# Kernel optimization log

Measured on AMD Instinct MI355X. Metric: run time of the kernel, lower is better.

## Reference

```python
import jax, jax.numpy as jnp
import numpy as np


def setup_inputs() -> dict:
    key = jax.random.key(0)
    k1, k2, k3, k4 = jax.random.split(key, 4)
    N, K, F, E = 50000, 32, 128, 16
    nodes = jax.random.normal(k1, (N, F), dtype=jnp.float32)
    nlist = jax.random.randint(k2, (N, K), 0, N, dtype=jnp.int64)
    edges = jax.random.uniform(k3, (N, K, E), dtype=jnp.float32)
    w = jax.random.normal(k4, (F, F, E), dtype=jnp.float32) * 0.05
    return {"nodes": nodes, "nlist": nlist, "edges": edges, "w": w}


def reference(nodes, nlist, edges, w):
    # gather neighbor features: [N, K, F]
    sliced = nodes[nlist]
    K = nlist.shape[1]
    # fused 3-way contraction + mean over neighbors (axis j):
    # original: einsum('ijn,ijl,lmn->ijm', edges, sliced, w).mean(axis=1)
    out = jnp.einsum('ijn,ijl,lmn->im', edges, sliced, w) / K
    return out
```

## Files before the change

kernel.cpp:

```cpp
#include <hip/hip_runtime.h>


typedef _Float16 half8  __attribute__((ext_vector_type(8)));
typedef _Float16 half4v __attribute__((ext_vector_type(4)));
typedef float    float4v __attribute__((ext_vector_type(4)));
typedef int      int4v  __attribute__((ext_vector_type(4)));
typedef unsigned int uint;

#define NF 128
#define NK 32
#define NE 16
#define RPB 32

__global__ __launch_bounds__(256) void k_prep_nodes(const float* __restrict__ src,
                                                    _Float16* __restrict__ dst, int n4) {
    int i = blockIdx.x * 256 + threadIdx.x;
    if (i < n4) {
        float4v v = ((const float4v*)src)[i];
        half4v h;
        h[0] = (_Float16)v[0]; h[1] = (_Float16)v[1];
        h[2] = (_Float16)v[2]; h[3] = (_Float16)v[3];
        ((half4v*)dst)[i] = h;
    }
}

__global__ __launch_bounds__(256) void k_prep_w(const float* __restrict__ w,
                                                _Float16* __restrict__ w2t) {
    int o  = blockIdx.x * 256 + threadIdx.x;
    int m  = o >> 11;
    int cf = o & 2047;
    int ch = cf >> 9;
    int cp = cf & 511;
    int ltq = cp >> 6;
    int n   = (cp >> 2) & 15;
    int g   = cp & 3;
    int l = ch * 32 + (ltq >> 2) * 16 + (ltq & 3) * 4 + g;
    w2t[o] = (_Float16)w[(l * NF + m) * NE + n];
}

__global__ __launch_bounds__(256, 4) void k_mp(const _Float16* __restrict__ nodes_h,
                                               const int* __restrict__ nlist,
                                               const float* __restrict__ edges,
                                               const _Float16* __restrict__ w2t,
                                               float* __restrict__ out, int N) {
    __shared__ __align__(16) _Float16 s_T[RPB * 512];
    __shared__ __align__(16) _Float16 s_G[4 * NK * 32];

    const int tid  = threadIdx.x;
    const int wv   = tid >> 6;
    const int ln   = tid & 63;
    const int quad = ln >> 4;
    const int c16  = ln & 15;
    const int row0 = blockIdx.x * RPB;

    _Float16* __restrict__ gbuf = &s_G[wv * (NK * 32)];
    const float4v zf = {0.f, 0.f, 0.f, 0.f};

    half8 fe[8];
    #pragma unroll
    for (int r = 0; r < 8; ++r) {
        int rg = row0 + wv * 8 + r; if (rg > N - 1) rg = N - 1;
        const float* ep = edges + (size_t)rg * (NK * NE) + quad * (8 * NE) + c16;
        #pragma unroll
        for (int jj = 0; jj < 8; ++jj) fe[r][jj] = (_Float16)ep[jj * NE];
    }

    const int jlane = ln >> 2;
    const int sub   = ln & 3;
    int nb0[8], nb1[8];
    #pragma unroll
    for (int r = 0; r < 8; ++r) {
        int rg = row0 + wv * 8 + r; if (rg > N - 1) rg = N - 1;
        nb0[r] = nlist[rg * NK + jlane]      << 8;
        nb1[r] = nlist[rg * NK + 16 + jlane] << 8;
    }
    const int wblk0 = (sub ^ ((jlane >> 3) & 3)) << 3;
    const int wblk1 = (sub ^ (((jlane + 16) >> 3) & 3)) << 3;

    float4v a00 = zf, a01 = zf, a10 = zf, a11 = zf;
    const char* nbase = (const char*)nodes_h;

    half8 p0 = *(const half8*)(nbase + nb0[0] + sub * 16);
    half8 p1 = *(const half8*)(nbase + nb1[0] + sub * 16);

    for (int ch = 0; ch < 4; ++ch) {
        #pragma unroll
        for (int r = 0; r < 8; ++r) {
            const int il = wv * 8 + r;
            half8 g0 = p0;
            half8 g1 = p1;
            if (r < 7) {
                p0 = *(const half8*)(nbase + nb0[r + 1] + ch * 64 + sub * 16);
                p1 = *(const half8*)(nbase + nb1[r + 1] + ch * 64 + sub * 16);
            }
            *(half8*)&gbuf[jlane * 32 + wblk0]        = g0;
            *(half8*)&gbuf[(jlane + 16) * 32 + wblk1] = g1;
            #pragma unroll
            for (int lt = 0; lt < 2; ++lt) {
                const int col   = lt * 16 + c16;
                const int rbase = quad * (8 * 32) + (col ^ (quad << 3));
                uint t0 = *(const unsigned short*)&gbuf[rbase + 0 * 32];
                uint t1 = *(const unsigned short*)&gbuf[rbase + 1 * 32];
                uint t2 = *(const unsigned short*)&gbuf[rbase + 2 * 32];
                uint t3 = *(const unsigned short*)&gbuf[rbase + 3 * 32];
                uint t4 = *(const unsigned short*)&gbuf[rbase + 4 * 32];
                uint t5 = *(const unsigned short*)&gbuf[rbase + 5 * 32];
                uint t6 = *(const unsigned short*)&gbuf[rbase + 6 * 32];
                uint t7 = *(const unsigned short*)&gbuf[rbase + 7 * 32];
                int4v pv;
                pv[0] = (int)(t0 | (t1 << 16));
                pv[1] = (int)(t2 | (t3 << 16));
                pv[2] = (int)(t4 | (t5 << 16));
                pv[3] = (int)(t6 | (t7 << 16));
                half8 av = __builtin_bit_cast(half8, pv);
                float4v d = __builtin_amdgcn_mfma_f32_16x16x32_f16(av, fe[r], zf, 0, 0, 0);
                const int ltq  = lt * 4 + quad;
                const int cb   = ltq * 64 + c16 * 4;
                const int phys = cb ^ ((((ltq ^ il) & 7)) << 3);
                half4v hv;
                hv[0] = (_Float16)d[0]; hv[1] = (_Float16)d[1];
                hv[2] = (_Float16)d[2]; hv[3] = (_Float16)d[3];
                *(half4v*)&s_T[il * 512 + phys] = hv;
            }
        }
        __syncthreads();

        if (ch < 3) {
            p0 = *(const half8*)(nbase + nb0[0] + (ch + 1) * 64 + sub * 16);
            p1 = *(const half8*)(nbase + nb1[0] + (ch + 1) * 64 + sub * 16);
        }

        const _Float16* wr0 = w2t + ((size_t)(wv * 2 + 0) * 16 + c16) * 2048 + ch * 512;
        const _Float16* wr1 = w2t + ((size_t)(wv * 2 + 1) * 16 + c16) * 2048 + ch * 512;
        #pragma unroll 4
        for (int kt = 0; kt < 16; ++kt) {
            const int cb2  = kt * 32 + quad * 8;
            const int mask = (((cb2 >> 6) ^ c16) & 7) << 3;
            half8 t0 = *(const half8*)&s_T[c16 * 512        + (cb2 ^ mask)];
            half8 t1 = *(const half8*)&s_T[(16 + c16) * 512 + (cb2 ^ mask)];
            half8 b0 = *(const half8*)(wr0 + cb2);
            half8 b1 = *(const half8*)(wr1 + cb2);
            a00 = __builtin_amdgcn_mfma_f32_16x16x32_f16(t0, b0, a00, 0, 0, 0);
            a10 = __builtin_amdgcn_mfma_f32_16x16x32_f16(t1, b0, a10, 0, 0, 0);
            a01 = __builtin_amdgcn_mfma_f32_16x16x32_f16(t0, b1, a01, 0, 0, 0);
            a11 = __builtin_amdgcn_mfma_f32_16x16x32_f16(t1, b1, a11, 0, 0, 0);
        }
        __syncthreads();
    }

    const float sc = 1.0f / (float)NK;
    const int mb = (wv << 5) + c16;
    #pragma unroll
    for (int g = 0; g < 4; ++g) {
        int i0 = row0 + quad * 4 + g;
        int i1 = i0 + 16;
        if (i0 < N) {
            out[(size_t)i0 * NF + mb]      = a00[g] * sc;
            out[(size_t)i0 * NF + mb + 16] = a01[g] * sc;
        }
        if (i1 < N) {
            out[(size_t)i1 * NF + mb]      = a10[g] * sc;
            out[(size_t)i1 * NF + mb + 16] = a11[g] * sc;
        }
    }
}

extern "C" void kernel_launch(void* const* d_in, const int* in_sizes, int n_in,
                              void* d_out, int out_size, void* d_ws, size_t ws_size,
                              hipStream_t stream) {
    const float* nodes = (const float*)d_in[0];
    const int*   nlist = (const int*)d_in[1];
    const float* edges = (const float*)d_in[2];
    const float* w     = (const float*)d_in[3];
    float* out = (float*)d_out;

    const int N = in_sizes[0] / NF;

    _Float16* w2t     = (_Float16*)d_ws;
    _Float16* nodes_h = (_Float16*)((char*)d_ws + 524288);

    const int n4 = (N * NF) / 4;
    k_prep_nodes<<<(n4 + 255) / 256, 256, 0, stream>>>(nodes, nodes_h, n4);
    k_prep_w<<<(NF * NF * NE) / 256, 256, 0, stream>>>(w, w2t);

    const int blocks = (N + RPB - 1) / RPB;
    k_mp<<<blocks, 256, 0, stream>>>(nodes_h, nlist, edges, w2t, out, N);
}
```

Baseline: 334.9 us.

## Halve rows per block, widen feature chunks, and stage output through LDS

The fused gather/MFMA kernel now handles 16 rows per block instead of 32. It processes features in two 64-wide chunks instead of four 32-wide chunks, with the weight reorder kernel changed to match. The gather layout moves to 8 lanes per neighbour row with four loads in flight, and the second-stage GEMM loop doubles in length with half the accumulators. Output goes through shared memory for coalesced float4 stores. This reduces barriers and gives more blocks for load balance, but each block reads the weight matrix for half as many rows, which doubles weight traffic per output. Occupancy hint drops to 3 blocks per CU.

```diff
diff --git a/kernel.cpp b/kernel.cpp
--- a/kernel.cpp
+++ b/kernel.cpp
@@ -10,7 +10,7 @@
 #define NF 128
 #define NK 32
 #define NE 16
-#define RPB 32
+#define RPB 16
 
 __global__ __launch_bounds__(256) void k_prep_nodes(const float* __restrict__ src,
                                                     _Float16* __restrict__ dst, int n4) {
@@ -26,25 +26,25 @@
 
 __global__ __launch_bounds__(256) void k_prep_w(const float* __restrict__ w,
                                                 _Float16* __restrict__ w2t) {
-    int o  = blockIdx.x * 256 + threadIdx.x;
-    int m  = o >> 11;
-    int cf = o & 2047;
-    int ch = cf >> 9;
-    int cp = cf & 511;
+    int o   = blockIdx.x * 256 + threadIdx.x;
+    int m   = o >> 11;
+    int cf  = o & 2047;
+    int ch  = cf >> 10;
+    int cp  = cf & 1023;
     int ltq = cp >> 6;
     int n   = (cp >> 2) & 15;
     int g   = cp & 3;
-    int l = ch * 32 + (ltq >> 2) * 16 + (ltq & 3) * 4 + g;
+    int l = ch * 64 + (ltq >> 2) * 16 + (ltq & 3) * 4 + g;
     w2t[o] = (_Float16)w[(l * NF + m) * NE + n];
 }
 
-__global__ __launch_bounds__(256, 4) void k_mp(const _Float16* __restrict__ nodes_h,
+__global__ __launch_bounds__(256, 3) void k_mp(const _Float16* __restrict__ nodes_h,
                                                const int* __restrict__ nlist,
                                                const float* __restrict__ edges,
                                                const _Float16* __restrict__ w2t,
                                                float* __restrict__ out, int N) {
-    __shared__ __align__(16) _Float16 s_T[RPB * 512];
-    __shared__ __align__(16) _Float16 s_G[4 * NK * 32];
+    __shared__ __align__(16) _Float16 s_T[RPB * 1024];
+    __shared__ __align__(16) _Float16 s_G[4 * 2048];
 
     const int tid  = threadIdx.x;
     const int wv   = tid >> 6;
@@ -53,60 +53,72 @@
     const int c16  = ln & 15;
     const int row0 = blockIdx.x * RPB;
 
-    _Float16* __restrict__ gbuf = &s_G[wv * (NK * 32)];
+    _Float16* __restrict__ gbuf = &s_G[wv * 2048];
     const float4v zf = {0.f, 0.f, 0.f, 0.f};
 
-    half8 fe[8];
-    #pragma unroll
-    for (int r = 0; r < 8; ++r) {
-        int rg = row0 + wv * 8 + r; if (rg > N - 1) rg = N - 1;
+    half8 fe[4];
+    #pragma unroll
+    for (int r = 0; r < 4; ++r) {
+        int rg = row0 + wv * 4 + r; if (rg > N - 1) rg = N - 1;
         const float* ep = edges + (size_t)rg * (NK * NE) + quad * (8 * NE) + c16;
         #pragma unroll
         for (int jj = 0; jj < 8; ++jj) fe[r][jj] = (_Float16)ep[jj * NE];
     }
 
-    const int jlane = ln >> 2;
-    const int sub   = ln & 3;
-    int nb0[8], nb1[8];
-    #pragma unroll
-    for (int r = 0; r < 8; ++r) {
-        int rg = row0 + wv * 8 + r; if (rg > N - 1) rg = N - 1;
-        nb0[r] = nlist[rg * NK + jlane]      << 8;
-        nb1[r] = nlist[rg * NK + 16 + jlane] << 8;
-    }
-    const int wblk0 = (sub ^ ((jlane >> 3) & 3)) << 3;
-    const int wblk1 = (sub ^ (((jlane + 16) >> 3) & 3)) << 3;
-
-    float4v a00 = zf, a01 = zf, a10 = zf, a11 = zf;
-    const char* nbase = (const char*)nodes_h;
-
-    half8 p0 = *(const half8*)(nbase + nb0[0] + sub * 16);
-    half8 p1 = *(const half8*)(nbase + nb1[0] + sub * 16);
-
-    for (int ch = 0; ch < 4; ++ch) {
+    const int jrow = ln >> 3;
+    const int s8   = ln & 7;
+    int nb0[4], nb1[4], nb2[4], nb3[4];
+    #pragma unroll
+    for (int r = 0; r < 4; ++r) {
+        int rg = row0 + wv * 4 + r; if (rg > N - 1) rg = N - 1;
+        const int* np = nlist + rg * NK + jrow;
+        nb0[r] = np[0]  << 8;
+        nb1[r] = np[8]  << 8;
+        nb2[r] = np[16] << 8;
+        nb3[r] = np[24] << 8;
+    }
+    const char* nbase = (const char*)nodes_h + (s8 << 4);
+
+    const int wo0 = (0 * 8 + jrow) * 64 + ((s8 ^ 0) << 3);
+    const int wo1 = (1 * 8 + jrow) * 64 + ((s8 ^ 1) << 3);
+    const int wo2 = (2 * 8 + jrow) * 64 + ((s8 ^ 2) << 3);
+    const int wo3 = (3 * 8 + jrow) * 64 + ((s8 ^ 3) << 3);
+
+    float4v a00 = zf, a01 = zf;
+
+    half8 pf0 = *(const half8*)(nbase + nb0[0]);
+    half8 pf1 = *(const half8*)(nbase + nb1[0]);
+    half8 pf2 = *(const half8*)(nbase + nb2[0]);
+    half8 pf3 = *(const half8*)(nbase + nb3[0]);
+
+    for (int ch = 0; ch < 2; ++ch) {
+        const int chb = ch << 7;
+
         #pragma unroll
-        for (int r = 0; r < 8; ++r) {
-            const int il = wv * 8 + r;
-            half8 g0 = p0;
-            half8 g1 = p1;
-            if (r < 7) {
-                p0 = *(const half8*)(nbase + nb0[r + 1] + ch * 64 + sub * 16);
-                p1 = *(const half8*)(nbase + nb1[r + 1] + ch * 64 + sub * 16);
+        for (int r = 0; r < 4; ++r) {
+            half8 g0 = pf0, g1 = pf1, g2 = pf2, g3 = pf3;
+            if (r < 3) {
+                pf0 = *(const half8*)(nbase + nb0[r + 1] + chb);
+                pf1 = *(const half8*)(nbase + nb1[r + 1] + chb);
+                pf2 = *(const half8*)(nbase + nb2[r + 1] + chb);
+                pf3 = *(const half8*)(nbase + nb3[r + 1] + chb);
             }
-            *(half8*)&gbuf[jlane * 32 + wblk0]        = g0;
-            *(half8*)&gbuf[(jlane + 16) * 32 + wblk1] = g1;
+            *(half8*)&gbuf[wo0] = g0;
+            *(half8*)&gbuf[wo1] = g1;
+            *(half8*)&gbuf[wo2] = g2;
+            *(half8*)&gbuf[wo3] = g3;
+            const int il = wv * 4 + r;
             #pragma unroll
-            for (int lt = 0; lt < 2; ++lt) {
-                const int col   = lt * 16 + c16;
-                const int rbase = quad * (8 * 32) + (col ^ (quad << 3));
-                uint t0 = *(const unsigned short*)&gbuf[rbase + 0 * 32];
-                uint t1 = *(const unsigned short*)&gbuf[rbase + 1 * 32];
-                uint t2 = *(const unsigned short*)&gbuf[rbase + 2 * 32];
-                uint t3 = *(const unsigned short*)&gbuf[rbase + 3 * 32];
-                uint t4 = *(const unsigned short*)&gbuf[rbase + 4 * 32];
-                uint t5 = *(const unsigned short*)&gbuf[rbase + 5 * 32];
-                uint t6 = *(const unsigned short*)&gbuf[rbase + 6 * 32];
-                uint t7 = *(const unsigned short*)&gbuf[rbase + 7 * 32];
+            for (int lt = 0; lt < 4; ++lt) {
+                const int rbase = quad * 512 + ((lt * 16 + c16) ^ (quad << 3));
+                uint t0 = *(const unsigned short*)&gbuf[rbase + 0 * 64];
+                uint t1 = *(const unsigned short*)&gbuf[rbase + 1 * 64];
+                uint t2 = *(const unsigned short*)&gbuf[rbase + 2 * 64];
+                uint t3 = *(const unsigned short*)&gbuf[rbase + 3 * 64];
+                uint t4 = *(const unsigned short*)&gbuf[rbase + 4 * 64];
+                uint t5 = *(const unsigned short*)&gbuf[rbase + 5 * 64];
+                uint t6 = *(const unsigned short*)&gbuf[rbase + 6 * 64];
+                uint t7 = *(const unsigned short*)&gbuf[rbase + 7 * 64];
                 int4v pv;
                 pv[0] = (int)(t0 | (t1 << 16));
                 pv[1] = (int)(t2 | (t3 << 16));
@@ -116,52 +128,52 @@
                 float4v d = __builtin_amdgcn_mfma_f32_16x16x32_f16(av, fe[r], zf, 0, 0, 0);
                 const int ltq  = lt * 4 + quad;
                 const int cb   = ltq * 64 + c16 * 4;
-                const int phys = cb ^ ((((ltq ^ il) & 7)) << 3);
+                const int phys = cb ^ (((ltq ^ il) & 7) << 3);
                 half4v hv;
                 hv[0] = (_Float16)d[0]; hv[1] = (_Float16)d[1];
                 hv[2] = (_Float16)d[2]; hv[3] = (_Float16)d[3];
-                *(half4v*)&s_T[il * 512 + phys] = hv;
+                *(half4v*)&s_T[il * 1024 + phys] = hv;
             }
         }
         __syncthreads();
 
-        if (ch < 3) {
-            p0 = *(const half8*)(nbase + nb0[0] + (ch + 1) * 64 + sub * 16);
-            p1 = *(const half8*)(nbase + nb1[0] + (ch + 1) * 64 + sub * 16);
+        if (ch == 0) {
+            pf0 = *(const half8*)(nbase + nb0[0] + 128);
+            pf1 = *(const half8*)(nbase + nb1[0] + 128);
+            pf2 = *(const half8*)(nbase + nb2[0] + 128);
+            pf3 = *(const half8*)(nbase + nb3[0] + 128);
         }
 
-        const _Float16* wr0 = w2t + ((size_t)(wv * 2 + 0) * 16 + c16) * 2048 + ch * 512;
-        const _Float16* wr1 = w2t + ((size_t)(wv * 2 + 1) * 16 + c16) * 2048 + ch * 512;
+        const _Float16* wr0 = w2t + ((size_t)(wv * 2 + 0) * 16 + c16) * 2048 + ch * 1024;
+        const _Float16* wr1 = w2t + ((size_t)(wv * 2 + 1) * 16 + c16) * 2048 + ch * 1024;
         #pragma unroll 4
-        for (int kt = 0; kt < 16; ++kt) {
+        for (int kt = 0; kt < 32; ++kt) {
             const int cb2  = kt * 32 + quad * 8;
             const int mask = (((cb2 >> 6) ^ c16) & 7) << 3;
-            half8 t0 = *(const half8*)&s_T[c16 * 512        + (cb2 ^ mask)];
-            half8 t1 = *(const half8*)&s_T[(16 + c16) * 512 + (cb2 ^ mask)];
+            half8 t0 = *(const half8*)&s_T[c16 * 1024 + (cb2 ^ mask)];
             half8 b0 = *(const half8*)(wr0 + cb2);
             half8 b1 = *(const half8*)(wr1 + cb2);
             a00 = __builtin_amdgcn_mfma_f32_16x16x32_f16(t0, b0, a00, 0, 0, 0);
-            a10 = __builtin_amdgcn_mfma_f32_16x16x32_f16(t1, b0, a10, 0, 0, 0);
             a01 = __builtin_amdgcn_mfma_f32_16x16x32_f16(t0, b1, a01, 0, 0, 0);
-            a11 = __builtin_amdgcn_mfma_f32_16x16x32_f16(t1, b1, a11, 0, 0, 0);
         }
         __syncthreads();
     }
 
+    float* sf = (float*)s_T;
     const float sc = 1.0f / (float)NK;
     const int mb = (wv << 5) + c16;
     #pragma unroll
     for (int g = 0; g < 4; ++g) {
-        int i0 = row0 + quad * 4 + g;
-        int i1 = i0 + 16;
-        if (i0 < N) {
-            out[(size_t)i0 * NF + mb]      = a00[g] * sc;
-            out[(size_t)i0 * NF + mb + 16] = a01[g] * sc;
-        }
-        if (i1 < N) {
-            out[(size_t)i1 * NF + mb]      = a10[g] * sc;
-            out[(size_t)i1 * NF + mb + 16] = a11[g] * sc;
-        }
+        sf[(quad * 4 + g) * NF + mb]      = a00[g] * sc;
+        sf[(quad * 4 + g) * NF + mb + 16] = a01[g] * sc;
+    }
+    __syncthreads();
+    const int lim = (N - row0) * NF;
+    float* ob = out + (size_t)row0 * NF;
+    #pragma unroll
+    for (int u = 0; u < 2; ++u) {
+        const int idx = (tid + u * 256) * 4;
+        if (idx < lim) *(float4v*)&ob[idx] = *(const float4v*)&sf[idx];
     }
 }
 
```

Result: slower. 369.1 us (+10.2%).
